# Kernel optimization log

Measured on AMD Instinct MI355X. Metric: run time of the kernel, lower is better.

Reference implementation:

```python
import jax, jax.numpy as jnp
import numpy as np


def _interp_linear(c, out_len):
    """PyTorch F.interpolate(mode='linear', align_corners=False) along last axis.
    c: (d, in_len) -> (d, out_len). Half-pixel coordinate mapping."""
    in_len = c.shape[-1]
    scale = in_len / out_len
    src = (jnp.arange(out_len, dtype=jnp.float32) + 0.5) * scale - 0.5
    src = jnp.clip(src, 0.0, in_len - 1)
    lo = jnp.floor(src).astype(jnp.int32)
    hi = jnp.minimum(lo + 1, in_len - 1)
    w = (src - lo.astype(jnp.float32)).astype(c.dtype)
    return c[..., lo] * (1.0 - w) + c[..., hi] * w


def _causal_spectrum(spec, fft_size):
    """Given the real part of a causal kernel's spectrum (1, F, d) with
    F = fft_size//2+1, recover the full complex spectrum via the Hilbert
    transform (analytic-signal window in time domain)."""
    t = jnp.fft.irfft(spec, n=fft_size, axis=1)  # even real kernel (1, fft_size, d)
    w = jnp.ones((fft_size,), dtype=t.dtype)
    w = w.at[1:fft_size // 2].set(2.0)
    w = w.at[fft_size // 2 + 1:].set(0.0)
    return jnp.fft.rfft(t * w[None, :, None], axis=1)  # (1, F, d) complex


def setup_inputs() -> dict:
    key = jax.random.key(0)
    k1, k2 = jax.random.split(key)
    B, N, D, NUM_FREQS = 8, 8192, 512, 512
    x = jax.random.normal(k1, (B, N, D), dtype=jnp.float32)
    coeffs = jax.random.normal(k2, (D, NUM_FREQS), dtype=jnp.float32)
    dc = jnp.ones((D, 1), dtype=jnp.float32)
    return {"x": x, "coeffs": coeffs, "dc": dc}


def reference(x, coeffs, dc):
    n = x.shape[-2]
    fft_size = int(2 ** int(np.ceil(np.log2(2 * n))))
    # interpolate learned real frequency coefficients up to fft_size//2 bins
    pos = _interp_linear(coeffs, fft_size // 2)          # (d, fft_size//2)
    a = jnp.concatenate([dc, pos], axis=1)               # (d, fft_size//2+1)
    a = jnp.transpose(a)[None]                           # (1, F, d)
    spec = _causal_spectrum(a, fft_size)                 # (1, F, d) complex
    xf = jnp.fft.rfft(x, n=fft_size, axis=-2)            # (B, F, d)
    out = jnp.fft.irfft(xf * spec, n=fft_size, axis=-2)  # (B, fft_size, d)
    return out[..., :n, :]
```

## Files before the change

kernel.cpp:

```cpp
#include <hip/hip_runtime.h>


#define FFT_M 8192
#define SPEC_LEN 8193

constexpr float PI_F = 3.14159265358979323846f;

__device__ __forceinline__ int swz(int k) {
    return k ^ (((k >> 4) ^ (k >> 8) ^ (k >> 12)) & 15);
}

__device__ __forceinline__ int rev13(int k) {
    int d1 = k & 3, d2 = (k >> 2) & 3, d3 = (k >> 4) & 3, d4 = (k >> 6) & 1;
    int d5 = (k >> 7) & 3, d6 = (k >> 9) & 3, d7 = (k >> 11) & 3;
    return (d1 << 11) | (d2 << 9) | (d3 << 7) | (d4 << 6) | (d5 << 4) | (d6 << 2) | d7;
}

__device__ __forceinline__ float2 cmul(float2 a, float2 b) {
    return make_float2(a.x * b.x - a.y * b.y, a.x * b.y + a.y * b.x);
}

template <int L>
__device__ void r4stage(float2* s, int tid, float sign) {
    constexpr float invL = 1.0f / (float)L;
    #pragma unroll
    for (int t = 0; t < 4; ++t) {
        int j = tid + t * 512;
        int pos = j & (L - 1);
        int blk = j - pos;
        int i0 = 4 * blk + pos;
        float2 a  = s[swz(i0)];
        float2 b  = s[swz(i0 + L)];
        float2 c  = s[swz(i0 + 2 * L)];
        float2 dd = s[swz(i0 + 3 * L)];
        float th = sign * (PI_F * 0.5f) * (float)pos * invL;
        float sn, cs;
        __sincosf(th, &sn, &cs);
        float2 w1 = make_float2(cs, sn);
        float2 w2 = cmul(w1, w1);
        float2 w3 = cmul(w2, w1);
        b = cmul(b, w1); c = cmul(c, w2); dd = cmul(dd, w3);
        float2 t0 = make_float2(a.x + c.x, a.y + c.y);
        float2 t1 = make_float2(a.x - c.x, a.y - c.y);
        float2 t2 = make_float2(b.x + dd.x, b.y + dd.y);
        float2 t3 = make_float2(b.x - dd.x, b.y - dd.y);
        float2 j3 = make_float2(-sign * t3.y, sign * t3.x);
        s[swz(i0)]         = make_float2(t0.x + t2.x, t0.y + t2.y);
        s[swz(i0 + L)]     = make_float2(t1.x + j3.x, t1.y + j3.y);
        s[swz(i0 + 2 * L)] = make_float2(t0.x - t2.x, t0.y - t2.y);
        s[swz(i0 + 3 * L)] = make_float2(t1.x - j3.x, t1.y - j3.y);
    }
    __syncthreads();
}

__device__ void r2stage(float2* s, int tid, float sign) {
    #pragma unroll
    for (int t = 0; t < 8; ++t) {
        int j = tid + t * 512;
        int pos = j & 63;
        int blk = j - pos;
        int i0 = 2 * blk + pos;
        float2 a = s[swz(i0)];
        float2 b = s[swz(i0 + 64)];
        float sn, cs;
        __sincosf(sign * (PI_F / 64.0f) * (float)pos, &sn, &cs);
        float2 wb = cmul(b, make_float2(cs, sn));
        s[swz(i0)]      = make_float2(a.x + wb.x, a.y + wb.y);
        s[swz(i0 + 64)] = make_float2(a.x - wb.x, a.y - wb.y);
    }
    __syncthreads();
}

__device__ void fft8192(float2* s, int tid, float sign) {
    #pragma unroll
    for (int t = 0; t < 16; ++t) {
        int k = tid + t * 512;
        int r = rev13(k);
        if (r > k) {
            float2 a = s[swz(k)];
            float2 b = s[swz(r)];
            s[swz(k)] = b;
            s[swz(r)] = a;
        }
    }
    __syncthreads();
    r4stage<1>(s, tid, sign);
    r4stage<4>(s, tid, sign);
    r4stage<16>(s, tid, sign);
    r2stage(s, tid, sign);
    r4stage<128>(s, tid, sign);
    r4stage<512>(s, tid, sign);
    r4stage<2048>(s, tid, sign);
}

__device__ __forceinline__ float aval(const float* C, float dcv, int idx) {
    if (idx == 0) return dcv;
    int j = idx - 1;
    float src = ((float)j + 0.5f) * 0.0625f - 0.5f;
    src = fminf(fmaxf(src, 0.0f), 511.0f);
    int lo = (int)floorf(src);
    int hi = min(lo + 1, 511);
    float w = src - (float)lo;
    return C[lo] * (1.0f - w) + C[hi] * w;
}

__global__ __launch_bounds__(512) void k0_spec(const float* __restrict__ coeffs,
                                               const float* __restrict__ dc,
                                               float2* __restrict__ spec) {
    __shared__ float2 sbuf[FFT_M];
    int d = blockIdx.x;
    int tid = threadIdx.x;
    const float* C = coeffs + d * 512;
    float dcv = dc[d];
    #pragma unroll
    for (int t = 0; t < 16; ++t) {
        int k = tid + t * 512;
        float ak = aval(C, dcv, k);
        float am = aval(C, dcv, 8192 - k);
        float Ae = 0.5f * (ak + am);
        float Ao = 0.5f * (ak - am);
        float sn, cs;
        __sincosf((PI_F / 8192.0f) * (float)k, &sn, &cs);
        sbuf[swz(k)] = make_float2(Ae - Ao * sn, Ao * cs);
    }
    __syncthreads();
    fft8192(sbuf, tid, 1.0f);
    #pragma unroll
    for (int t = 0; t < 16; ++t) {
        int n = tid + t * 512;
        float2 z = sbuf[swz(n)];
        float te = z.x * (1.0f / 8192.0f);
        float to = z.y * (1.0f / 8192.0f);
        int m0 = 2 * n;
        float he = (m0 == 0) ? te : ((m0 < 8192) ? 2.0f * te : ((m0 == 8192) ? te : 0.0f));
        float ho = (m0 + 1 < 8192) ? 2.0f * to : 0.0f;
        sbuf[swz(n)] = make_float2(he, ho);
    }
    __syncthreads();
    fft8192(sbuf, tid, -1.0f);
    float2* Sd = spec + (size_t)d * SPEC_LEN;
    const float scale = 1.0f / 8192.0f;
    #pragma unroll
    for (int t = 0; t < 8; ++t) {
        int k = tid + t * 512;
        if (k == 0) {
            float2 Z0 = sbuf[swz(0)];
            Sd[0]    = make_float2((Z0.x + Z0.y) * scale, 0.0f);
            Sd[8192] = make_float2((Z0.x - Z0.y) * scale, 0.0f);
            float2 Z4 = sbuf[swz(4096)];
            Sd[4096] = make_float2(Z4.x * scale, -Z4.y * scale);
        } else {
            int km = 8192 - k;
            float2 Zk = sbuf[swz(k)];
            float2 Zm = sbuf[swz(km)];
            float2 Xe = make_float2((Zk.x + Zm.x) * 0.5f, (Zk.y - Zm.y) * 0.5f);
            float2 dz = make_float2((Zk.x - Zm.x) * 0.5f, (Zk.y + Zm.y) * 0.5f);
            float2 Xo = make_float2(dz.y, -dz.x);
            float sn, cs;
            __sincosf(-(PI_F / 8192.0f) * (float)k, &sn, &cs);
            float2 wXo = cmul(make_float2(cs, sn), Xo);
            Sd[k]  = make_float2((Xe.x + wXo.x) * scale, (Xe.y + wXo.y) * scale);
            Sd[km] = make_float2((Xe.x - wXo.x) * scale, -(Xe.y - wXo.y) * scale);
        }
    }
}

__global__ __launch_bounds__(256) void k1_pack(const float* __restrict__ x,
                                               float2* __restrict__ zin) {
    __shared__ float tile[64][33];
    int bb = blockIdx.z;
    int nt = blockIdx.x;
    int dt = blockIdx.y;
    int tx = threadIdx.x & 31, ty = threadIdx.x >> 5;
    const float* xb = x + (size_t)bb * 8192 * 512;
    int n0 = nt * 64;
    int d0 = dt * 32;
    #pragma unroll
    for (int r = 0; r < 8; ++r) {
        int row = ty + r * 8;
        tile[row][tx] = xb[(size_t)(n0 + row) * 512 + d0 + tx];
    }
    __syncthreads();
    #pragma unroll
    for (int r = 0; r < 4; ++r) {
        int dl = ty + r * 8;
        int d  = d0 + dl;
        int np = nt * 32 + tx;
        float2 v = make_float2(tile[2 * tx][dl], tile[2 * tx + 1][dl]);
        zin[((size_t)(d * 8 + bb)) * 4096 + np] = v;
    }
}

__global__ __launch_bounds__(512) void k2_conv(const float2* zin,
                                               const float2* __restrict__ spec,
                                               float2* yout) {
    __shared__ float2 sbuf[FFT_M];
    int wg = blockIdx.x;
    int d = wg >> 3;
    int tid = threadIdx.x;
    const float2* zi = zin + (size_t)wg * 4096;
    #pragma unroll
    for (int t = 0; t < 8; ++t) {
        int n = tid + t * 512;
        sbuf[swz(n)] = zi[n];
        sbuf[swz(n + 4096)] = make_float2(0.0f, 0.0f);
    }
    __syncthreads();
    fft8192(sbuf, tid, -1.0f);
    const float2* S = spec + (size_t)d * SPEC_LEN;
    #pragma unroll
    for (int t = 0; t < 8; ++t) {
        int k = tid + t * 512;
        if (k == 0) {
            float2 Z0 = sbuf[swz(0)];
            float X0 = Z0.x + Z0.y;
            float XM = Z0.x - Z0.y;
            float2 S0 = S[0], SM = S[8192];
            float2 Y0 = make_float2(X0 * S0.x, X0 * S0.y);
            float2 YM = make_float2(XM * SM.x, XM * SM.y);
            float2 Ye = make_float2((Y0.x + YM.x) * 0.5f, (Y0.y - YM.y) * 0.5f);
            float2 Yo = make_float2((Y0.x - YM.x) * 0.5f, (Y0.y + YM.y) * 0.5f);
            sbuf[swz(0)] = make_float2(Ye.x - Yo.y, Ye.y + Yo.x);
            float2 Z4 = sbuf[swz(4096)];
            float2 Y4 = cmul(make_float2(Z4.x, -Z4.y), S[4096]);
            sbuf[swz(4096)] = make_float2(Y4.x, -Y4.y);
        } else {
            int km = 8192 - k;
            float2 Zk = sbuf[swz(k)];
            float2 Zm = sbuf[swz(km)];
            float2 Xe = make_float2((Zk.x + Zm.x) * 0.5f, (Zk.y - Zm.y) * 0.5f);
            float2 dz = make_float2((Zk.x - Zm.x) * 0.5f, (Zk.y + Zm.y) * 0.5f);
            float2 Xo = make_float2(dz.y, -dz.x);
            float sn, cs;
            __sincosf(-(PI_F / 8192.0f) * (float)k, &sn, &cs);
            float2 w = make_float2(cs, sn);
            float2 wXo = cmul(w, Xo);
            float2 Xk = make_float2(Xe.x + wXo.x, Xe.y + wXo.y);
            float2 Xm = make_float2(Xe.x - wXo.x, -(Xe.y - wXo.y));
            float2 Yk = cmul(Xk, S[k]);
            float2 Ym = cmul(Xm, S[km]);
            float2 Ye = make_float2((Yk.x + Ym.x) * 0.5f, (Yk.y - Ym.y) * 0.5f);
            float2 dy = make_float2((Yk.x - Ym.x) * 0.5f, (Yk.y + Ym.y) * 0.5f);
            float2 Yo = cmul(make_float2(cs, -sn), dy);
            sbuf[swz(k)]  = make_float2(Ye.x - Yo.y, Ye.y + Yo.x);
            sbuf[swz(km)] = make_float2(Ye.x + Yo.y, Yo.x - Ye.y);
        }
    }
    __syncthreads();
    fft8192(sbuf, tid, 1.0f);
    float2* yo = yout + (size_t)wg * 4096;
    #pragma unroll
    for (int t = 0; t < 8; ++t) {
        int n = tid + t * 512;
        yo[n] = sbuf[swz(n)];
    }
}

__global__ __launch_bounds__(256) void k3_unpack(const float2* __restrict__ yout,
                                                 float* __restrict__ out) {
    __shared__ float2 tile[32][33];
    int bb = blockIdx.z, nt = blockIdx.x, dt = blockIdx.y;
    int tx = threadIdx.x & 31, ty = threadIdx.x >> 5;
    int d0 = dt * 32, np0 = nt * 32;
    #pragma unroll
    for (int r = 0; r < 4; ++r) {
        int dl = ty + r * 8;
        tile[dl][tx] = yout[((size_t)((d0 + dl) * 8 + bb)) * 4096 + np0 + tx];
    }
    __syncthreads();
    float* ob = out + (size_t)bb * 8192 * 512;
    #pragma unroll
    for (int r = 0; r < 4; ++r) {
        int nl = ty + r * 8;
        int n  = np0 + nl;
        float2 v = tile[tx][nl];
        ob[(size_t)(2 * n) * 512 + d0 + tx]     = v.x;
        ob[(size_t)(2 * n + 1) * 512 + d0 + tx] = v.y;
    }
}

extern "C" void kernel_launch(void* const* d_in, const int* in_sizes, int n_in,
                              void* d_out, int out_size, void* d_ws, size_t ws_size,
                              hipStream_t stream) {
    const float* x      = (const float*)d_in[0];
    const float* coeffs = (const float*)d_in[1];
    const float* dc     = (const float*)d_in[2];
    float* out = (float*)d_out;

    float2* spec = (float2*)d_ws;
    float2* zbuf = (float2*)((char*)d_ws + (size_t)512 * SPEC_LEN * sizeof(float2));

    k0_spec<<<512, 512, 0, stream>>>(coeffs, dc, spec);
    k1_pack<<<dim3(128, 16, 8), 256, 0, stream>>>(x, zbuf);
    k2_conv<<<4096, 512, 0, stream>>>(zbuf, spec, zbuf);
    k3_unpack<<<dim3(128, 16, 8), 256, 0, stream>>>(zbuf, out);
}
```

Measured before the change: 593.3 us.

## Replace radix-4 shared-memory FFT with register-resident 16x16x32 decomposition and merge kernels

Replaces the bit-reversal plus seven shared-memory radix stages with a three-level decomposition (radix-16, radix-16, radix-32 split across lane pairs). The butterflies run in registers, use constant twiddles, and use skewed shared-memory addressing. This cuts LDS passes, barriers and sincos calls per FFT. k2 skips the zero half of the padded input and the unused output half directly in registers. It also fuses the spectrum and pack kernels into one launch and widens the pack/unpack transposes to float4 accesses, at the cost of more register pressure and much more complex indexing.

```diff
diff --git a/kernel.cpp b/kernel.cpp
--- a/kernel.cpp
+++ b/kernel.cpp
@@ -1,96 +1,175 @@
 #include <hip/hip_runtime.h>
 
 
-#define FFT_M 8192
 #define SPEC_LEN 8193
-
 constexpr float PI_F = 3.14159265358979323846f;
 
-__device__ __forceinline__ int swz(int k) {
-    return k ^ (((k >> 4) ^ (k >> 8) ^ (k >> 12)) & 15);
-}
-
-__device__ __forceinline__ int rev13(int k) {
-    int d1 = k & 3, d2 = (k >> 2) & 3, d3 = (k >> 4) & 3, d4 = (k >> 6) & 1;
-    int d5 = (k >> 7) & 3, d6 = (k >> 9) & 3, d7 = (k >> 11) & 3;
-    return (d1 << 11) | (d2 << 9) | (d3 << 7) | (d4 << 6) | (d5 << 4) | (d6 << 2) | d7;
-}
-
+__device__ __forceinline__ float2 f2add(float2 a, float2 b) { return make_float2(a.x + b.x, a.y + b.y); }
+__device__ __forceinline__ float2 f2sub(float2 a, float2 b) { return make_float2(a.x - b.x, a.y - b.y); }
 __device__ __forceinline__ float2 cmul(float2 a, float2 b) {
     return make_float2(a.x * b.x - a.y * b.y, a.x * b.y + a.y * b.x);
 }
 
-template <int L>
-__device__ void r4stage(float2* s, int tid, float sign) {
-    constexpr float invL = 1.0f / (float)L;
-    #pragma unroll
-    for (int t = 0; t < 4; ++t) {
-        int j = tid + t * 512;
-        int pos = j & (L - 1);
-        int blk = j - pos;
-        int i0 = 4 * blk + pos;
-        float2 a  = s[swz(i0)];
-        float2 b  = s[swz(i0 + L)];
-        float2 c  = s[swz(i0 + 2 * L)];
-        float2 dd = s[swz(i0 + 3 * L)];
-        float th = sign * (PI_F * 0.5f) * (float)pos * invL;
-        float sn, cs;
-        __sincosf(th, &sn, &cs);
-        float2 w1 = make_float2(cs, sn);
-        float2 w2 = cmul(w1, w1);
-        float2 w3 = cmul(w2, w1);
-        b = cmul(b, w1); c = cmul(c, w2); dd = cmul(dd, w3);
-        float2 t0 = make_float2(a.x + c.x, a.y + c.y);
-        float2 t1 = make_float2(a.x - c.x, a.y - c.y);
-        float2 t2 = make_float2(b.x + dd.x, b.y + dd.y);
-        float2 t3 = make_float2(b.x - dd.x, b.y - dd.y);
-        float2 j3 = make_float2(-sign * t3.y, sign * t3.x);
-        s[swz(i0)]         = make_float2(t0.x + t2.x, t0.y + t2.y);
-        s[swz(i0 + L)]     = make_float2(t1.x + j3.x, t1.y + j3.y);
-        s[swz(i0 + 2 * L)] = make_float2(t0.x - t2.x, t0.y - t2.y);
-        s[swz(i0 + 3 * L)] = make_float2(t1.x - j3.x, t1.y - j3.y);
-    }
-    __syncthreads();
-}
-
-__device__ void r2stage(float2* s, int tid, float sign) {
-    #pragma unroll
-    for (int t = 0; t < 8; ++t) {
-        int j = tid + t * 512;
-        int pos = j & 63;
-        int blk = j - pos;
-        int i0 = 2 * blk + pos;
-        float2 a = s[swz(i0)];
-        float2 b = s[swz(i0 + 64)];
-        float sn, cs;
-        __sincosf(sign * (PI_F / 64.0f) * (float)pos, &sn, &cs);
-        float2 wb = cmul(b, make_float2(cs, sn));
-        s[swz(i0)]      = make_float2(a.x + wb.x, a.y + wb.y);
-        s[swz(i0 + 64)] = make_float2(a.x - wb.x, a.y - wb.y);
-    }
-    __syncthreads();
-}
-
-__device__ void fft8192(float2* s, int tid, float sign) {
-    #pragma unroll
-    for (int t = 0; t < 16; ++t) {
-        int k = tid + t * 512;
-        int r = rev13(k);
-        if (r > k) {
-            float2 a = s[swz(k)];
-            float2 b = s[swz(r)];
-            s[swz(k)] = b;
-            s[swz(r)] = a;
-        }
-    }
-    __syncthreads();
-    r4stage<1>(s, tid, sign);
-    r4stage<4>(s, tid, sign);
-    r4stage<16>(s, tid, sign);
-    r2stage(s, tid, sign);
-    r4stage<128>(s, tid, sign);
-    r4stage<512>(s, tid, sign);
-    r4stage<2048>(s, tid, sign);
+#define SLOT(k) ((((k) & 3) << 2) | ((k) >> 2))
+
+__device__ __forceinline__ int addr1(int n2, int k1) {
+    return (n2 << 4) | ((k1 + n2) & 15);
+}
+__device__ __forceinline__ int addr2(int r, int m2) {
+    return (r << 5) | ((m2 + 2 * r) & 31);
+}
+__device__ __forceinline__ int addr3(int k) {
+    int lo = (k + 2 * (k >> 4) + (k >> 8) + (k >> 12)) & 15;
+    return (k & ~15) | lo;
+}
+
+template <int SGN>
+__device__ __forceinline__ void fft4(float2& a, float2& b, float2& c, float2& d) {
+    float2 A0 = f2add(a, c), A1 = f2sub(a, c), A2 = f2add(b, d), A3 = f2sub(b, d);
+    float2 T = (SGN < 0) ? make_float2(A3.y, -A3.x) : make_float2(-A3.y, A3.x);
+    a = f2add(A0, A2); b = f2add(A1, T); c = f2sub(A0, A2); d = f2sub(A1, T);
+}
+
+template <int SGN>
+__device__ __forceinline__ void fft16_tail(float2* v) {
+    const float C1 = 0.9238795325112867f, S1 = 0.3826834323650898f, R2 = 0.7071067811865476f;
+    v[5]  = cmul(v[5],  make_float2(C1, SGN < 0 ? -S1 : S1));
+    v[6]  = cmul(v[6],  make_float2(R2, SGN < 0 ? -R2 : R2));
+    v[7]  = cmul(v[7],  make_float2(S1, SGN < 0 ? -C1 : C1));
+    v[9]  = cmul(v[9],  make_float2(R2, SGN < 0 ? -R2 : R2));
+    v[10] = (SGN < 0) ? make_float2(v[10].y, -v[10].x) : make_float2(-v[10].y, v[10].x);
+    v[11] = cmul(v[11], make_float2(-R2, SGN < 0 ? -R2 : R2));
+    v[13] = cmul(v[13], make_float2(S1, SGN < 0 ? -C1 : C1));
+    v[14] = cmul(v[14], make_float2(-R2, SGN < 0 ? -R2 : R2));
+    v[15] = cmul(v[15], make_float2(-C1, SGN < 0 ? S1 : -S1));
+    fft4<SGN>(v[0], v[1], v[2], v[3]);
+    fft4<SGN>(v[4], v[5], v[6], v[7]);
+    fft4<SGN>(v[8], v[9], v[10], v[11]);
+    fft4<SGN>(v[12], v[13], v[14], v[15]);
+}
+template <int SGN>
+__device__ __forceinline__ void fft16(float2* v) {
+    fft4<SGN>(v[0], v[4], v[8], v[12]);
+    fft4<SGN>(v[1], v[5], v[9], v[13]);
+    fft4<SGN>(v[2], v[6], v[10], v[14]);
+    fft4<SGN>(v[3], v[7], v[11], v[15]);
+    fft16_tail<SGN>(v);
+}
+template <int SGN>
+__device__ __forceinline__ void fft16_half(float2* v) {
+    #pragma unroll
+    for (int j = 0; j < 4; ++j) {
+        float2 a = v[j], b = v[j + 4];
+        float2 T = (SGN < 0) ? make_float2(b.y, -b.x) : make_float2(-b.y, b.x);
+        v[j] = f2add(a, b); v[j + 4] = f2add(a, T);
+        v[j + 8] = f2sub(a, b); v[j + 12] = f2sub(a, T);
+    }
+    fft16_tail<SGN>(v);
+}
+
+__device__ __forceinline__ void twchain(float2* v, float2 w) {
+    float2 acc = w;
+    v[SLOT(1)] = cmul(v[SLOT(1)], acc);
+    #pragma unroll
+    for (int k = 2; k < 16; ++k) { acc = cmul(acc, w); v[SLOT(k)] = cmul(v[SLOT(k)], acc); }
+}
+__device__ __forceinline__ void twchain_nat(float2* v, float2 w) {
+    float2 acc = w;
+    v[1] = cmul(v[1], acc);
+    #pragma unroll
+    for (int k = 2; k < 16; ++k) { acc = cmul(acc, w); v[k] = cmul(v[k], acc); }
+}
+
+__device__ __forceinline__ float2 shflx1(float2 v) {
+    return make_float2(__shfl_xor(v.x, 1), __shfl_xor(v.y, 1));
+}
+
+#define W32_TABLES \
+    constexpr float WC[16] = {1.f, 0.98078528f, 0.92387953f, 0.83146961f, 0.70710678f, \
+        0.55557023f, 0.38268343f, 0.19509032f, 0.f, -0.19509032f, -0.38268343f, \
+        -0.55557023f, -0.70710678f, -0.83146961f, -0.92387953f, -0.98078528f}; \
+    constexpr float WS[16] = {0.f, 0.19509032f, 0.38268343f, 0.55557023f, 0.70710678f, \
+        0.83146961f, 0.92387953f, 0.98078528f, 1.f, 0.98078528f, 0.92387953f, \
+        0.83146961f, 0.70710678f, 0.55557023f, 0.38268343f, 0.19509032f};
+
+__device__ __forceinline__ void fwd_L2_L3(float2* sbuf, int tid) {
+    {
+        int k1 = tid >> 5, m2 = tid & 31;
+        float2 u[16];
+        #pragma unroll
+        for (int m1 = 0; m1 < 16; ++m1) u[m1] = sbuf[addr1(32 * m1 + m2, k1)];
+        __syncthreads();
+        fft16<-1>(u);
+        float sn, cs; __sincosf(-(PI_F / 256.0f) * (float)m2, &sn, &cs);
+        twchain(u, make_float2(cs, sn));
+        #pragma unroll
+        for (int q1 = 0; q1 < 16; ++q1) sbuf[addr2(k1 * 16 + q1, m2)] = u[SLOT(q1)];
+        __syncthreads();
+    }
+    {
+        int k1 = tid >> 5, q1 = (tid >> 1) & 15, half = tid & 1;
+        float2 e[16];
+        #pragma unroll
+        for (int j = 0; j < 16; ++j) e[j] = sbuf[addr2(k1 * 16 + q1, 2 * j + half)];
+        __syncthreads();
+        fft16<-1>(e);
+        W32_TABLES
+        #pragma unroll
+        for (int q = 0; q < 16; ++q) {
+            float2 mine = e[SLOT(q)];
+            float2 othr = shflx1(mine);
+            float2 Eq = half ? othr : mine;
+            float2 Oq = half ? mine : othr;
+            float2 WO = cmul(make_float2(WC[q], -WS[q]), Oq);
+            float2 X = half ? f2sub(Eq, WO) : f2add(Eq, WO);
+            int k = k1 + 16 * q1 + 256 * (q + 16 * half);
+            sbuf[addr3(k)] = X;
+        }
+        __syncthreads();
+    }
+}
+
+__device__ __forceinline__ void inv_L3_L2(float2* sbuf, int tid) {
+    {
+        int k1 = tid >> 5, q1 = (tid >> 1) & 15, half = tid & 1;
+        float2 t[16];
+        #pragma unroll
+        for (int q = 0; q < 16; ++q)
+            t[q] = sbuf[addr3(k1 + 16 * q1 + 256 * (q + 16 * half))];
+        __syncthreads();
+        W32_TABLES
+        #pragma unroll
+        for (int q = 0; q < 16; ++q) {
+            float2 othr = shflx1(t[q]);
+            if (half) t[q] = cmul(make_float2(WC[q], WS[q]), f2sub(othr, t[q]));
+            else      t[q] = f2add(t[q], othr);
+        }
+        fft16<1>(t);
+        #pragma unroll
+        for (int j = 0; j < 16; ++j) sbuf[addr2(k1 * 16 + q1, 2 * j + half)] = t[SLOT(j)];
+        __syncthreads();
+    }
+    {
+        int k1 = tid >> 5, m2 = tid & 31;
+        float2 u[16];
+        #pragma unroll
+        for (int q1 = 0; q1 < 16; ++q1) u[q1] = sbuf[addr2(k1 * 16 + q1, m2)];
+        __syncthreads();
+        float sn, cs; __sincosf((PI_F / 256.0f) * (float)m2, &sn, &cs);
+        twchain_nat(u, make_float2(cs, sn));
+        fft16<1>(u);
+        #pragma unroll
+        for (int m1 = 0; m1 < 16; ++m1) sbuf[addr1(32 * m1 + m2, k1)] = u[SLOT(m1)];
+        __syncthreads();
+    }
+}
+
+__device__ __forceinline__ void inv_L1(const float2* sbuf, int tid, float2* v) {
+    #pragma unroll
+    for (int k1 = 0; k1 < 16; ++k1) v[k1] = sbuf[addr1(tid, k1)];
+    float sn, cs; __sincosf((PI_F / 4096.0f) * (float)tid, &sn, &cs);
+    twchain_nat(v, make_float2(cs, sn));
+    fft16<1>(v);
 }
 
 __device__ __forceinline__ float aval(const float* C, float dcv, int idx) {
@@ -104,178 +183,196 @@
     return C[lo] * (1.0f - w) + C[hi] * w;
 }
 
-__global__ __launch_bounds__(512) void k0_spec(const float* __restrict__ coeffs,
-                                               const float* __restrict__ dc,
-                                               float2* __restrict__ spec) {
-    __shared__ float2 sbuf[FFT_M];
-    int d = blockIdx.x;
+__global__ __launch_bounds__(512) void k01(const float* __restrict__ x,
+                                           const float* __restrict__ coeffs,
+                                           const float* __restrict__ dc,
+                                           float2* __restrict__ spec,
+                                           float2* __restrict__ zin) {
+    __shared__ float2 sbuf[8192];
     int tid = threadIdx.x;
-    const float* C = coeffs + d * 512;
-    float dcv = dc[d];
-    #pragma unroll
-    for (int t = 0; t < 16; ++t) {
-        int k = tid + t * 512;
-        float ak = aval(C, dcv, k);
-        float am = aval(C, dcv, 8192 - k);
-        float Ae = 0.5f * (ak + am);
-        float Ao = 0.5f * (ak - am);
-        float sn, cs;
-        __sincosf((PI_F / 8192.0f) * (float)k, &sn, &cs);
-        sbuf[swz(k)] = make_float2(Ae - Ao * sn, Ao * cs);
-    }
+    if (blockIdx.x < 512) {
+        int d = blockIdx.x;
+        const float* C = coeffs + d * 512;
+        float dcv = dc[d];
+        #pragma unroll
+        for (int tt = 0; tt < 16; ++tt) {
+            int k = tid + (tt << 9);
+            float ak = aval(C, dcv, k);
+            float am = aval(C, dcv, 8192 - k);
+            float Ae = 0.5f * (ak + am), Ao = 0.5f * (ak - am);
+            float sn, cs; __sincosf((PI_F / 8192.0f) * (float)k, &sn, &cs);
+            sbuf[addr3(k)] = make_float2(Ae - Ao * sn, Ao * cs);
+        }
+        __syncthreads();
+        inv_L3_L2(sbuf, tid);
+        float2 v[16];
+        inv_L1(sbuf, tid, v);
+        float2 u[16];
+        #pragma unroll
+        for (int n1 = 0; n1 < 16; ++n1) {
+            float2 z = v[SLOT(n1)];
+            int n = (n1 << 9) + tid;
+            float te = z.x * (1.0f / 8192.0f);
+            float to = z.y * (1.0f / 8192.0f);
+            int m0 = 2 * n;
+            float he = (m0 == 0) ? te : ((m0 < 8192) ? 2.0f * te : ((m0 == 8192) ? te : 0.0f));
+            float ho = (m0 + 1 < 8192) ? 2.0f * to : 0.0f;
+            u[n1] = make_float2(he, ho);
+        }
+        fft16<-1>(u);
+        float sn, cs; __sincosf(-(PI_F / 4096.0f) * (float)tid, &sn, &cs);
+        twchain(u, make_float2(cs, sn));
+        #pragma unroll
+        for (int k1 = 0; k1 < 16; ++k1) sbuf[addr1(tid, k1)] = u[SLOT(k1)];
+        __syncthreads();
+        fwd_L2_L3(sbuf, tid);
+        float2* Sd = spec + (size_t)d * SPEC_LEN;
+        const float scale = 1.0f / 8192.0f;
+        #pragma unroll
+        for (int tt = 0; tt < 8; ++tt) {
+            int k = tid + (tt << 9);
+            if (k == 0) {
+                float2 Z0 = sbuf[addr3(0)];
+                Sd[0]    = make_float2((Z0.x + Z0.y) * scale, 0.0f);
+                Sd[8192] = make_float2((Z0.x - Z0.y) * scale, 0.0f);
+                float2 Z4 = sbuf[addr3(4096)];
+                Sd[4096] = make_float2(Z4.x * scale, -Z4.y * scale);
+            } else {
+                int km = 8192 - k;
+                float2 Zk = sbuf[addr3(k)], Zm = sbuf[addr3(km)];
+                float2 Xe = make_float2((Zk.x + Zm.x) * 0.5f, (Zk.y - Zm.y) * 0.5f);
+                float2 dz = make_float2((Zk.x - Zm.x) * 0.5f, (Zk.y + Zm.y) * 0.5f);
+                float2 Xo = make_float2(dz.y, -dz.x);
+                float sn2, cs2; __sincosf(-(PI_F / 8192.0f) * (float)k, &sn2, &cs2);
+                float2 wXo = cmul(make_float2(cs2, sn2), Xo);
+                Sd[k]  = make_float2((Xe.x + wXo.x) * scale, (Xe.y + wXo.y) * scale);
+                Sd[km] = make_float2((Xe.x - wXo.x) * scale, -(Xe.y - wXo.y) * scale);
+            }
+        }
+    } else {
+        int bid = blockIdx.x - 512;
+        int nt = bid & 127, dt = (bid >> 7) & 7, bb = bid >> 10;
+        float* tile = (float*)sbuf;
+        const float4* x4 = (const float4*)(x + ((size_t)bb * 8192 + (size_t)nt * 64) * 512 + dt * 64);
+        int lane4 = tid & 15, row = tid >> 4;
+        #pragma unroll
+        for (int r = 0; r < 2; ++r) {
+            int rr = row + 32 * r;
+            float4 vv = x4[(size_t)rr * 128 + lane4];
+            float* dst = &tile[rr * 65 + lane4 * 4];
+            dst[0] = vv.x; dst[1] = vv.y; dst[2] = vv.z; dst[3] = vv.w;
+        }
+        __syncthreads();
+        int tx4 = tid & 15, dl = tid >> 4;
+        #pragma unroll
+        for (int r = 0; r < 2; ++r) {
+            int dloc = dl + 32 * r;
+            int d = dt * 64 + dloc;
+            int npb = nt * 32 + 2 * tx4;
+            float4 w;
+            w.x = tile[(4 * tx4 + 0) * 65 + dloc];
+            w.y = tile[(4 * tx4 + 1) * 65 + dloc];
+            w.z = tile[(4 * tx4 + 2) * 65 + dloc];
+            w.w = tile[(4 * tx4 + 3) * 65 + dloc];
+            *(float4*)&zin[((size_t)(d * 8 + bb)) * 4096 + npb] = w;
+        }
+    }
+}
+
+__global__ __launch_bounds__(512) void k2_conv(const float2* __restrict__ zin,
+                                               const float2* __restrict__ spec,
+                                               float2* __restrict__ yout) {
+    __shared__ float2 sbuf[8192];
+    int wg = blockIdx.x, d = wg >> 3, tid = threadIdx.x;
+    const float2* zi = zin + (size_t)wg * 4096;
+    float2 v[16];
+    #pragma unroll
+    for (int n1 = 0; n1 < 8; ++n1) v[n1] = zi[(n1 << 9) + tid];
+    fft16_half<-1>(v);
+    {
+        float sn, cs; __sincosf(-(PI_F / 4096.0f) * (float)tid, &sn, &cs);
+        twchain(v, make_float2(cs, sn));
+    }
+    #pragma unroll
+    for (int k1 = 0; k1 < 16; ++k1) sbuf[addr1(tid, k1)] = v[SLOT(k1)];
     __syncthreads();
-    fft8192(sbuf, tid, 1.0f);
-    #pragma unroll
-    for (int t = 0; t < 16; ++t) {
-        int n = tid + t * 512;
-        float2 z = sbuf[swz(n)];
-        float te = z.x * (1.0f / 8192.0f);
-        float to = z.y * (1.0f / 8192.0f);
-        int m0 = 2 * n;
-        float he = (m0 == 0) ? te : ((m0 < 8192) ? 2.0f * te : ((m0 == 8192) ? te : 0.0f));
-        float ho = (m0 + 1 < 8192) ? 2.0f * to : 0.0f;
-        sbuf[swz(n)] = make_float2(he, ho);
-    }
-    __syncthreads();
-    fft8192(sbuf, tid, -1.0f);
-    float2* Sd = spec + (size_t)d * SPEC_LEN;
-    const float scale = 1.0f / 8192.0f;
-    #pragma unroll
-    for (int t = 0; t < 8; ++t) {
-        int k = tid + t * 512;
+    fwd_L2_L3(sbuf, tid);
+    const float2* S = spec + (size_t)d * SPEC_LEN;
+    #pragma unroll
+    for (int tt = 0; tt < 8; ++tt) {
+        int k = tid + (tt << 9);
         if (k == 0) {
-            float2 Z0 = sbuf[swz(0)];
-            Sd[0]    = make_float2((Z0.x + Z0.y) * scale, 0.0f);
-            Sd[8192] = make_float2((Z0.x - Z0.y) * scale, 0.0f);
-            float2 Z4 = sbuf[swz(4096)];
-            Sd[4096] = make_float2(Z4.x * scale, -Z4.y * scale);
-        } else {
-            int km = 8192 - k;
-            float2 Zk = sbuf[swz(k)];
-            float2 Zm = sbuf[swz(km)];
-            float2 Xe = make_float2((Zk.x + Zm.x) * 0.5f, (Zk.y - Zm.y) * 0.5f);
-            float2 dz = make_float2((Zk.x - Zm.x) * 0.5f, (Zk.y + Zm.y) * 0.5f);
-            float2 Xo = make_float2(dz.y, -dz.x);
-            float sn, cs;
-            __sincosf(-(PI_F / 8192.0f) * (float)k, &sn, &cs);
-            float2 wXo = cmul(make_float2(cs, sn), Xo);
-            Sd[k]  = make_float2((Xe.x + wXo.x) * scale, (Xe.y + wXo.y) * scale);
-            Sd[km] = make_float2((Xe.x - wXo.x) * scale, -(Xe.y - wXo.y) * scale);
-        }
-    }
-}
-
-__global__ __launch_bounds__(256) void k1_pack(const float* __restrict__ x,
-                                               float2* __restrict__ zin) {
-    __shared__ float tile[64][33];
-    int bb = blockIdx.z;
-    int nt = blockIdx.x;
-    int dt = blockIdx.y;
-    int tx = threadIdx.x & 31, ty = threadIdx.x >> 5;
-    const float* xb = x + (size_t)bb * 8192 * 512;
-    int n0 = nt * 64;
-    int d0 = dt * 32;
-    #pragma unroll
-    for (int r = 0; r < 8; ++r) {
-        int row = ty + r * 8;
-        tile[row][tx] = xb[(size_t)(n0 + row) * 512 + d0 + tx];
-    }
-    __syncthreads();
-    #pragma unroll
-    for (int r = 0; r < 4; ++r) {
-        int dl = ty + r * 8;
-        int d  = d0 + dl;
-        int np = nt * 32 + tx;
-        float2 v = make_float2(tile[2 * tx][dl], tile[2 * tx + 1][dl]);
-        zin[((size_t)(d * 8 + bb)) * 4096 + np] = v;
-    }
-}
-
-__global__ __launch_bounds__(512) void k2_conv(const float2* zin,
-                                               const float2* __restrict__ spec,
-                                               float2* yout) {
-    __shared__ float2 sbuf[FFT_M];
-    int wg = blockIdx.x;
-    int d = wg >> 3;
-    int tid = threadIdx.x;
-    const float2* zi = zin + (size_t)wg * 4096;
-    #pragma unroll
-    for (int t = 0; t < 8; ++t) {
-        int n = tid + t * 512;
-        sbuf[swz(n)] = zi[n];
-        sbuf[swz(n + 4096)] = make_float2(0.0f, 0.0f);
-    }
-    __syncthreads();
-    fft8192(sbuf, tid, -1.0f);
-    const float2* S = spec + (size_t)d * SPEC_LEN;
-    #pragma unroll
-    for (int t = 0; t < 8; ++t) {
-        int k = tid + t * 512;
-        if (k == 0) {
-            float2 Z0 = sbuf[swz(0)];
-            float X0 = Z0.x + Z0.y;
-            float XM = Z0.x - Z0.y;
+            float2 Z0 = sbuf[addr3(0)];
+            float X0 = Z0.x + Z0.y, XM = Z0.x - Z0.y;
             float2 S0 = S[0], SM = S[8192];
             float2 Y0 = make_float2(X0 * S0.x, X0 * S0.y);
             float2 YM = make_float2(XM * SM.x, XM * SM.y);
             float2 Ye = make_float2((Y0.x + YM.x) * 0.5f, (Y0.y - YM.y) * 0.5f);
             float2 Yo = make_float2((Y0.x - YM.x) * 0.5f, (Y0.y + YM.y) * 0.5f);
-            sbuf[swz(0)] = make_float2(Ye.x - Yo.y, Ye.y + Yo.x);
-            float2 Z4 = sbuf[swz(4096)];
+            sbuf[addr3(0)] = make_float2(Ye.x - Yo.y, Ye.y + Yo.x);
+            int p4 = addr3(4096);
+            float2 Z4 = sbuf[p4];
             float2 Y4 = cmul(make_float2(Z4.x, -Z4.y), S[4096]);
-            sbuf[swz(4096)] = make_float2(Y4.x, -Y4.y);
+            sbuf[p4] = make_float2(Y4.x, -Y4.y);
         } else {
             int km = 8192 - k;
-            float2 Zk = sbuf[swz(k)];
-            float2 Zm = sbuf[swz(km)];
+            int p1 = addr3(k), p2 = addr3(km);
+            float2 Zk = sbuf[p1], Zm = sbuf[p2];
             float2 Xe = make_float2((Zk.x + Zm.x) * 0.5f, (Zk.y - Zm.y) * 0.5f);
             float2 dz = make_float2((Zk.x - Zm.x) * 0.5f, (Zk.y + Zm.y) * 0.5f);
             float2 Xo = make_float2(dz.y, -dz.x);
-            float sn, cs;
-            __sincosf(-(PI_F / 8192.0f) * (float)k, &sn, &cs);
+            float sn, cs; __sincosf(-(PI_F / 8192.0f) * (float)k, &sn, &cs);
             float2 w = make_float2(cs, sn);
             float2 wXo = cmul(w, Xo);
-            float2 Xk = make_float2(Xe.x + wXo.x, Xe.y + wXo.y);
+            float2 Xk = f2add(Xe, wXo);
             float2 Xm = make_float2(Xe.x - wXo.x, -(Xe.y - wXo.y));
             float2 Yk = cmul(Xk, S[k]);
             float2 Ym = cmul(Xm, S[km]);
             float2 Ye = make_float2((Yk.x + Ym.x) * 0.5f, (Yk.y - Ym.y) * 0.5f);
             float2 dy = make_float2((Yk.x - Ym.x) * 0.5f, (Yk.y + Ym.y) * 0.5f);
             float2 Yo = cmul(make_float2(cs, -sn), dy);
-            sbuf[swz(k)]  = make_float2(Ye.x - Yo.y, Ye.y + Yo.x);
-            sbuf[swz(km)] = make_float2(Ye.x + Yo.y, Yo.x - Ye.y);
+            sbuf[p1] = make_float2(Ye.x - Yo.y, Ye.y + Yo.x);
+            sbuf[p2] = make_float2(Ye.x + Yo.y, Yo.x - Ye.y);
         }
     }
     __syncthreads();
-    fft8192(sbuf, tid, 1.0f);
+    inv_L3_L2(sbuf, tid);
+    inv_L1(sbuf, tid, v);
     float2* yo = yout + (size_t)wg * 4096;
     #pragma unroll
-    for (int t = 0; t < 8; ++t) {
-        int n = tid + t * 512;
-        yo[n] = sbuf[swz(n)];
-    }
-}
-
-__global__ __launch_bounds__(256) void k3_unpack(const float2* __restrict__ yout,
+    for (int n1 = 0; n1 < 8; ++n1) yo[(n1 << 9) + tid] = v[SLOT(n1)];
+}
+
+__global__ __launch_bounds__(512) void k3_unpack(const float2* __restrict__ yout,
                                                  float* __restrict__ out) {
-    __shared__ float2 tile[32][33];
-    int bb = blockIdx.z, nt = blockIdx.x, dt = blockIdx.y;
-    int tx = threadIdx.x & 31, ty = threadIdx.x >> 5;
-    int d0 = dt * 32, np0 = nt * 32;
-    #pragma unroll
-    for (int r = 0; r < 4; ++r) {
-        int dl = ty + r * 8;
-        tile[dl][tx] = yout[((size_t)((d0 + dl) * 8 + bb)) * 4096 + np0 + tx];
+    __shared__ float2 tile[64 * 33];
+    int bid = blockIdx.x;
+    int nt = bid & 127, dt = (bid >> 7) & 7, bb = bid >> 10;
+    int tid = threadIdx.x;
+    const float4* y4 = (const float4*)yout;
+    int tx4 = tid & 15, dl = tid >> 4;
+    #pragma unroll
+    for (int r = 0; r < 2; ++r) {
+        int dloc = dl + 32 * r;
+        int d = dt * 64 + dloc;
+        float4 vv = y4[(size_t)(d * 8 + bb) * 2048 + nt * 16 + tx4];
+        tile[dloc * 33 + 2 * tx4]     = make_float2(vv.x, vv.y);
+        tile[dloc * 33 + 2 * tx4 + 1] = make_float2(vv.z, vv.w);
     }
     __syncthreads();
-    float* ob = out + (size_t)bb * 8192 * 512;
-    #pragma unroll
-    for (int r = 0; r < 4; ++r) {
-        int nl = ty + r * 8;
-        int n  = np0 + nl;
-        float2 v = tile[tx][nl];
-        ob[(size_t)(2 * n) * 512 + d0 + tx]     = v.x;
-        ob[(size_t)(2 * n + 1) * 512 + d0 + tx] = v.y;
+    const float* tf = (const float*)tile;
+    int lane4 = tid & 15, nl = tid >> 4;
+    #pragma unroll
+    for (int r = 0; r < 2; ++r) {
+        int nloc = nl + 32 * r;
+        int npl = nloc >> 1, e = nloc & 1;
+        float4 w;
+        w.x = tf[((4 * lane4 + 0) * 33 + npl) * 2 + e];
+        w.y = tf[((4 * lane4 + 1) * 33 + npl) * 2 + e];
+        w.z = tf[((4 * lane4 + 2) * 33 + npl) * 2 + e];
+        w.w = tf[((4 * lane4 + 3) * 33 + npl) * 2 + e];
+        int n = nt * 64 + nloc;
+        *(float4*)&out[((size_t)bb * 8192 + n) * 512 + dt * 64 + lane4 * 4] = w;
     }
 }
 
@@ -290,8 +387,7 @@
     float2* spec = (float2*)d_ws;
     float2* zbuf = (float2*)((char*)d_ws + (size_t)512 * SPEC_LEN * sizeof(float2));
 
-    k0_spec<<<512, 512, 0, stream>>>(coeffs, dc, spec);
-    k1_pack<<<dim3(128, 16, 8), 256, 0, stream>>>(x, zbuf);
+    k01<<<512 + 8192, 512, 0, stream>>>(x, coeffs, dc, spec, zbuf);
     k2_conv<<<4096, 512, 0, stream>>>(zbuf, spec, zbuf);
-    k3_unpack<<<dim3(128, 16, 8), 256, 0, stream>>>(zbuf, out);
-}
+    k3_unpack<<<8192, 512, 0, stream>>>(zbuf, out);
+}
```

After: 529.1 us. 1.12x faster.
